# Optimization experiments

Measured on AMD Instinct MI355X. Metric: run time of the kernel, lower is better.

## Reference

```python
import jax, jax.numpy as jnp
import numpy as np

BUCKET_SIZE = 128
HEADS = 8
HEAD_DIM = 64
LOOK_BACKWARD = 1
LOOK_FORWARD = 0  # causal => no look forward
TOKEN_SELF_ATTN_VALUE = -50000.0


def look_around(x, backward, forward, pad_value):
    n = x.shape[1]
    pw = [(0, 0)] * x.ndim
    pw[1] = (backward, forward)
    px = jnp.pad(x, pw, constant_values=pad_value)
    return jnp.concatenate([px[:, i:i + n] for i in range(backward + forward + 1)], axis=2)


def shift(x):
    # relative-shift trick: (..., i, j) -> (..., i, j)
    *lead, i, j = x.shape
    x = jnp.concatenate([x, jnp.zeros((*lead, i, i), x.dtype)], axis=-1)
    l = i + j - 1
    x = x.reshape(*lead, i * (i + j))
    pad = (-x.shape[-1]) % l
    x = jnp.concatenate([x, jnp.zeros((*lead, pad), x.dtype)], axis=-1)
    x = x.reshape(*lead, -1, l)
    return x[..., :i, i - 1:]


def setup_inputs() -> dict:
    key = jax.random.key(0)
    kq, kk, kv, kr = jax.random.split(key, 4)
    B, H, T, E = 2, HEADS, 8192, HEAD_DIM
    q = jax.random.normal(kq, (B, H, T, E), dtype=jnp.float32)
    k = jax.random.normal(kk, (B, H, T, E), dtype=jnp.float32)
    v = jax.random.normal(kv, (B, H, T, E), dtype=jnp.float32)
    rel_weights = jax.random.normal(kr, (2 * BUCKET_SIZE, H, E), dtype=jnp.float32)
    return {"q": q, "k": k, "v": v, "rel_weights": rel_weights}


def reference(q, k, v, rel_weights):
    B, H, T, E = q.shape
    qm = q.reshape(B * H, T, E)
    km = k.reshape(B * H, T, E)
    vm = v.reshape(B * H, T, E)

    # shared_qk: l2-normalize keys (F.normalize with eps=1e-12)
    km = km / jnp.maximum(jnp.linalg.norm(km, axis=-1, keepdims=True), 1e-12)

    buckets = T // BUCKET_SIZE
    bq = qm.reshape(B * H, buckets, BUCKET_SIZE, E)
    bk = km.reshape(B * H, buckets, BUCKET_SIZE, E)
    bv = vm.reshape(B * H, buckets, BUCKET_SIZE, E)

    bk = look_around(bk, LOOK_BACKWARD, LOOK_FORWARD, -1.0)
    bv = look_around(bv, LOOK_BACKWARD, LOOK_FORWARD, -1.0)

    ticker = jnp.arange(T, dtype=q.dtype)
    bq_t = ticker.reshape(1, buckets, BUCKET_SIZE)
    bq_k = look_around(bq_t, LOOK_BACKWARD, LOOK_FORWARD, -1.0)

    scale = E ** -0.5
    dots = jnp.einsum('bnie,bnje->bnij', bq, bk) * scale

    # relative positional bias
    bq5 = bq.reshape(B, H, buckets, BUCKET_SIZE, E)
    emb = jnp.einsum('bhnid,jhd->bhnij', bq5, rel_weights) * scale
    dots = dots + shift(emb).reshape(dots.shape)

    mask_value = -jnp.finfo(dots.dtype).max
    # shared_qk: mask self-attention positions
    self_mask = bq_t[:, :, :, None] == bq_k[:, :, None, :]
    dots = jnp.where(self_mask, TOKEN_SELF_ATTN_VALUE, dots)
    # causal mask
    causal_mask = bq_t[:, :, :, None] < bq_k[:, :, None, :]
    dots = jnp.where(causal_mask, mask_value, dots)
    # look-around padding mask
    pad_mask = (bq_k == -1.0)[:, :, None, :]
    dots = jnp.where(pad_mask, mask_value, dots)

    attn = jax.nn.softmax(dots, axis=-1)
    out = jnp.einsum('bnij,bnje->bnie', attn, bv)
    return out.reshape(B, H, T, E)
```

## Files before the change

### kernel.cpp

```cpp
#include <hip/hip_runtime.h>
#include <hip/hip_bf16.h>
#include <float.h>

#define NHEAD 8

typedef __attribute__((ext_vector_type(8))) short bf16x8;
typedef __attribute__((ext_vector_type(4))) float f32x4;

struct US44 { ushort4 a, b; };

static __device__ __forceinline__ unsigned short bfb(float f) {
    __hip_bfloat16 h = __float2bfloat16(f);
    unsigned short u; __builtin_memcpy(&u, &h, 2); return u;
}
static __device__ __forceinline__ unsigned int pk2(float a, float b) {
    return (unsigned int)bfb(a) | ((unsigned int)bfb(b) << 16);
}
static __device__ __forceinline__ float bf2f_lo(unsigned int u) { return __uint_as_float(u << 16); }
static __device__ __forceinline__ float bf2f_hi(unsigned int u) { return __uint_as_float(u & 0xffff0000u); }

static __device__ __forceinline__ int swz64(int r, int c) {
    return (r << 6) + (c ^ ((r & 7) << 3));
}
static __device__ __forceinline__ int vIdx(int c, int kk) {
    return (c << 8) + (kk ^ ((c & 31) << 2));
}
static __device__ __forceinline__ int pIdx(int wv, int row, int col) {
    const int ch = (col >> 3) ^ (row & 3);
    return (wv * 16 + row) * 40 + ch * 8 + (col & 7);
}

static __device__ __forceinline__ f32x4 mfma16(bf16x8 a, bf16x8 b, f32x4 c) {
    return __builtin_amdgcn_mfma_f32_16x16x32_bf16(a, b, c, 0, 0, 0);
}

__global__ __launch_bounds__(512, 4)
void local_attn_kernel(const float* __restrict__ qg, const float* __restrict__ kg,
                       const float* __restrict__ vg, const float* __restrict__ rwg,
                       float* __restrict__ outg)
{
    __shared__ __align__(16) unsigned short sB[256 * 64];
    __shared__ __align__(16) unsigned short sV[64 * 256];
    __shared__ __align__(16) unsigned short sP[8 * 16 * 40];

    const int tid  = threadIdx.x;
    const int lane = tid & 63;
    const int wv   = tid >> 6;
    const int jl   = lane & 15;
    const int hi   = lane >> 4;

    const int lb = ((blockIdx.x & 7) << 7) + (blockIdx.x >> 3);
    const int bh = lb >> 6;
    const int n  = lb & 63;
    const int h  = bh & 7;

    const float scale = 0.125f;

    const float* Qp = qg + ((size_t)bh * 8192 + (size_t)n * 128) * 64;
    const float* Kp = kg + (size_t)bh * 8192 * 64 + ((long)n - 1) * 128 * 64;
    const float* Vp = vg + (size_t)bh * 8192 * 64 + ((long)n - 1) * 128 * 64;

    const int cr = tid >> 4;
    const int c0 = (tid & 15) << 2;

    #pragma unroll
    for (int pp = 0; pp < 8; ++pp) {
        const int row = pp * 32 + cr;
        f32x4 x = {0.f, 0.f, 0.f, 0.f};
        if (!(n == 0 && row < 128))
            x = *reinterpret_cast<const f32x4*>(Vp + row * 64 + c0);
        #pragma unroll
        for (int q = 0; q < 4; ++q)
            sV[vIdx(c0 + q, row)] = bfb(x[q]);
    }

    #pragma unroll
    for (int pp = 0; pp < 8; ++pp) {
        const int row = pp * 32 + cr;
        f32x4 x = {0.f, 0.f, 0.f, 0.f};
        if (!(n == 0 && row < 128))
            x = *reinterpret_cast<const f32x4*>(Kp + row * 64 + c0);
        float ss = x[0] * x[0] + x[1] * x[1] + x[2] * x[2] + x[3] * x[3];
        ss += __shfl_xor(ss, 1);
        ss += __shfl_xor(ss, 2);
        ss += __shfl_xor(ss, 4);
        ss += __shfl_xor(ss, 8);
        const float rn = 1.0f / fmaxf(sqrtf(ss), 1e-12f);
        ushort4 pkk = make_ushort4(bfb(x[0] * rn), bfb(x[1] * rn),
                                   bfb(x[2] * rn), bfb(x[3] * rn));
        *reinterpret_cast<ushort4*>(&sB[swz64(row, c0)]) = pkk;
    }

    uint2 rwu[8];
    #pragma unroll
    for (int pp = 0; pp < 8; ++pp) {
        const int row = pp * 32 + cr;
        const f32x4 x = *reinterpret_cast<const f32x4*>(rwg + ((size_t)row * NHEAD + h) * 64 + c0);
        rwu[pp] = make_uint2(pk2(x[0], x[1]), pk2(x[2], x[3]));
    }
    #pragma unroll
    for (int pp = 0; pp < 8; ++pp)
        asm volatile("" :: "v"(rwu[pp].x), "v"(rwu[pp].y));

    const int arow = wv * 16 + jl;
    const int kq0  = hi << 3;
    const float* qr = Qp + arow * 64 + kq0;
    const f32x4 qa = *reinterpret_cast<const f32x4*>(qr);
    const f32x4 qb = *reinterpret_cast<const f32x4*>(qr + 4);
    const f32x4 qc = *reinterpret_cast<const f32x4*>(qr + 32);
    const f32x4 qd = *reinterpret_cast<const f32x4*>(qr + 36);
    bf16x8 aq0, aq1;
    #pragma unroll
    for (int q = 0; q < 4; ++q) {
        aq0[q]     = (short)bfb(qa[q] * scale);
        aq0[q + 4] = (short)bfb(qb[q] * scale);
        aq1[q]     = (short)bfb(qc[q] * scale);
        aq1[q + 4] = (short)bfb(qd[q] * scale);
    }

    __syncthreads();

    const int ibase = wv * 16 + (hi << 2);
    const int tMax  = wv + 8;

    f32x4 dots[16] = {};
    __builtin_amdgcn_s_setprio(1);
    #pragma unroll
    for (int t = 0; t < 16; ++t) {
        if (t <= tMax) {
            const int rr = t * 16 + jl;
            const bf16x8 b0 = *reinterpret_cast<const bf16x8*>(&sB[swz64(rr, kq0)]);
            const bf16x8 b1 = *reinterpret_cast<const bf16x8*>(&sB[swz64(rr, 32 + kq0)]);
            f32x4 d = {0.f, 0.f, 0.f, 0.f};
            d = mfma16(aq0, b0, d);
            d = mfma16(aq1, b1, d);
            dots[t] = d;
        }
    }
    __builtin_amdgcn_s_setprio(0);

    __syncthreads();

    #pragma unroll
    for (int pp = 0; pp < 8; ++pp) {
        const int row = pp * 32 + cr;
        *reinterpret_cast<uint2*>(&sB[swz64(row, c0)]) = rwu[pp];
    }

    __syncthreads();

    const int cv0 = 4 * hi + 1, cv1 = 4 * hi + 2, cv2 = 4 * hi + 3, cv3 = 4 * hi + 4;
    const int sl0 = (hi << 4) | ((jl - cv0) & 15);
    const int sl1 = (hi << 4) | ((jl - cv1) & 15);
    const int sl2 = (hi << 4) | ((jl - cv2) & 15);
    const int sl3 = (hi << 4) | ((jl - cv3) & 15);
    const bool g0 = jl >= cv0, g1 = jl >= cv1, g2 = jl >= cv2, g3 = jl >= cv3;

    unsigned int cur01, cur23;
    {
        const int rr = (7 - wv) * 16 + jl;
        const bf16x8 b0 = *reinterpret_cast<const bf16x8*>(&sB[swz64(rr, kq0)]);
        const bf16x8 b1 = *reinterpret_cast<const bf16x8*>(&sB[swz64(rr, 32 + kq0)]);
        f32x4 e = {0.f, 0.f, 0.f, 0.f};
        e = mfma16(aq0, b0, e);
        e = mfma16(aq1, b1, e);
        cur01 = pk2(e[0], e[1]);
        cur23 = pk2(e[2], e[3]);
    }
    unsigned int lo0 = (unsigned int)__shfl((int)cur01, sl0);
    unsigned int lo1 = (unsigned int)__shfl((int)cur01, sl1);
    unsigned int lo2 = (unsigned int)__shfl((int)cur23, sl2);
    unsigned int lo3 = (unsigned int)__shfl((int)cur23, sl3);

    #pragma unroll
    for (int t = 0; t < 16; ++t) {
        if (t <= tMax) {
            unsigned int n01 = 0, n23 = 0;
            const int ts = t + 8 - wv;
            if (ts < 16) {
                const int rr = ts * 16 + jl;
                const bf16x8 b0 = *reinterpret_cast<const bf16x8*>(&sB[swz64(rr, kq0)]);
                const bf16x8 b1 = *reinterpret_cast<const bf16x8*>(&sB[swz64(rr, 32 + kq0)]);
                f32x4 e = {0.f, 0.f, 0.f, 0.f};
                e = mfma16(aq0, b0, e);
                e = mfma16(aq1, b1, e);
                n01 = pk2(e[0], e[1]);
                n23 = pk2(e[2], e[3]);
            }
            const unsigned int h0 = (unsigned int)__shfl((int)n01, sl0);
            const unsigned int h1 = (unsigned int)__shfl((int)n01, sl1);
            const unsigned int h2 = (unsigned int)__shfl((int)n23, sl2);
            const unsigned int h3 = (unsigned int)__shfl((int)n23, sl3);
            dots[t][0] += bf2f_lo(g0 ? h0 : lo0);
            dots[t][1] += bf2f_hi(g1 ? h1 : lo1);
            dots[t][2] += bf2f_lo(g2 ? h2 : lo2);
            dots[t][3] += bf2f_hi(g3 ? h3 : lo3);
            lo0 = h0; lo1 = h1; lo2 = h2; lo3 = h3;
        }
    }

    #pragma unroll
    for (int tt = 8; tt <= 15; ++tt) {
        if (tt == tMax) {
            #pragma unroll
            for (int r = 0; r < 4; ++r) {
                const int dd = 128 + jl - 4 * hi - r;
                float x = dots[tt][r];
                x = (dd == 128) ? -50.0f : x;
                x = (dd > 128) ? -3.0e38f : x;
                dots[tt][r] = x;
            }
        }
    }
    if (n == 0) {
        #pragma unroll
        for (int t = 0; t < 8; ++t)
            #pragma unroll
            for (int r = 0; r < 4; ++r)
                dots[t][r] = -3.0e38f;
    }

    float sm[4] = {0.f, 0.f, 0.f, 0.f};
    #pragma unroll
    for (int t = 0; t < 16; ++t) {
        if (t <= tMax) {
            #pragma unroll
            for (int r = 0; r < 4; ++r) {
                const float pe = __expf(dots[t][r]);
                dots[t][r] = pe;
                sm[r] += pe;
            }
        }
    }
    float rinv[4];
    #pragma unroll
    for (int r = 0; r < 4; ++r) {
        sm[r] += __shfl_xor(sm[r], 1);
        sm[r] += __shfl_xor(sm[r], 2);
        sm[r] += __shfl_xor(sm[r], 4);
        sm[r] += __shfl_xor(sm[r], 8);
        rinv[r] = 1.0f / sm[r];
    }

    f32x4 o[4] = {};
    #pragma unroll
    for (int pv = 0; pv < 8; ++pv) {
        if (2 * pv <= tMax) {
            #pragma unroll
            for (int tt = 0; tt < 2; ++tt) {
                const int t = 2 * pv + tt;
                #pragma unroll
                for (int r = 0; r < 4; ++r) {
                    unsigned short val = 0;
                    if (t <= tMax) val = bfb(dots[t][r]);
                    sP[pIdx(wv, 4 * hi + r, tt * 16 + jl)] = val;
                }
            }
            const bf16x8 pa = *reinterpret_cast<const bf16x8*>(&sP[pIdx(wv, jl, kq0)]);
            __builtin_amdgcn_s_setprio(1);
            #pragma unroll
            for (int ct = 0; ct < 4; ++ct) {
                const int c = ct * 16 + jl;
                const ushort4 v0 = *reinterpret_cast<const ushort4*>(&sV[vIdx(c, pv * 32 + kq0)]);
                const ushort4 v1 = *reinterpret_cast<const ushort4*>(&sV[vIdx(c, pv * 32 + kq0 + 4)]);
                const bf16x8 vb = __builtin_bit_cast(bf16x8, US44{v0, v1});
                o[ct] = mfma16(pa, vb, o[ct]);
            }
            __builtin_amdgcn_s_setprio(0);
        }
    }

    float* Op = outg + ((size_t)bh * 8192 + (size_t)n * 128) * 64;
    #pragma unroll
    for (int ct = 0; ct < 4; ++ct)
        #pragma unroll
        for (int r = 0; r < 4; ++r)
            Op[(ibase + r) * 64 + ct * 16 + jl] = o[ct][r] * rinv[r];
}

extern "C" void kernel_launch(void* const* d_in, const int* in_sizes, int n_in,
                              void* d_out, int out_size, void* d_ws, size_t ws_size,
                              hipStream_t stream) {
    const float* q  = (const float*)d_in[0];
    const float* k  = (const float*)d_in[1];
    const float* v  = (const float*)d_in[2];
    const float* rw = (const float*)d_in[3];
    float* out = (float*)d_out;
    local_attn_kernel<<<dim3(1024), dim3(512), 0, stream>>>(q, k, v, rw, out);
}
```

Before: 48.87 us.

## Process two consecutive buckets per block, reusing shared K/V window and rel weights

Each block now handles two adjacent query buckets, so the grid is halved. The second bucket's look-back K/V half is the first bucket's own K/V and the rel-weight registers are reused, so global loads and normalization per bucket shrink. The next bucket's K is prefetched into registers during the first bucket's softmax, and the V halves are addressed with an XOR phase instead of being copied. In exchange there are fewer blocks (512 on a large GPU), which lowers parallelism and occupancy, and there is more register pressure from the prefetch buffers.

```diff
diff --git a/kernel.cpp b/kernel.cpp
--- a/kernel.cpp
+++ b/kernel.cpp
@@ -49,46 +49,52 @@
     const int jl   = lane & 15;
     const int hi   = lane >> 4;
 
-    const int lb = ((blockIdx.x & 7) << 7) + (blockIdx.x >> 3);
-    const int bh = lb >> 6;
-    const int n  = lb & 63;
-    const int h  = bh & 7;
+    const int bid = blockIdx.x;
+    const int lb  = ((bid & 7) << 6) + (bid >> 3);
+    const int bh  = lb >> 5;
+    const int nb  = (lb & 31) << 1;
+    const int h   = bh & 7;
 
     const float scale = 0.125f;
-
-    const float* Qp = qg + ((size_t)bh * 8192 + (size_t)n * 128) * 64;
-    const float* Kp = kg + (size_t)bh * 8192 * 64 + ((long)n - 1) * 128 * 64;
-    const float* Vp = vg + (size_t)bh * 8192 * 64 + ((long)n - 1) * 128 * 64;
+    const size_t bhOff = (size_t)bh * 8192 * 64;
 
     const int cr = tid >> 4;
     const int c0 = (tid & 15) << 2;
 
-    #pragma unroll
-    for (int pp = 0; pp < 8; ++pp) {
-        const int row = pp * 32 + cr;
-        f32x4 x = {0.f, 0.f, 0.f, 0.f};
-        if (!(n == 0 && row < 128))
-            x = *reinterpret_cast<const f32x4*>(Vp + row * 64 + c0);
-        #pragma unroll
-        for (int q = 0; q < 4; ++q)
-            sV[vIdx(c0 + q, row)] = bfb(x[q]);
-    }
-
-    #pragma unroll
-    for (int pp = 0; pp < 8; ++pp) {
-        const int row = pp * 32 + cr;
-        f32x4 x = {0.f, 0.f, 0.f, 0.f};
-        if (!(n == 0 && row < 128))
-            x = *reinterpret_cast<const f32x4*>(Kp + row * 64 + c0);
-        float ss = x[0] * x[0] + x[1] * x[1] + x[2] * x[2] + x[3] * x[3];
-        ss += __shfl_xor(ss, 1);
-        ss += __shfl_xor(ss, 2);
-        ss += __shfl_xor(ss, 4);
-        ss += __shfl_xor(ss, 8);
-        const float rn = 1.0f / fmaxf(sqrtf(ss), 1e-12f);
-        ushort4 pkk = make_ushort4(bfb(x[0] * rn), bfb(x[1] * rn),
-                                   bfb(x[2] * rn), bfb(x[3] * rn));
-        *reinterpret_cast<ushort4*>(&sB[swz64(row, c0)]) = pkk;
+    const int arow  = wv * 16 + jl;
+    const int kq0   = hi << 3;
+    const int ibase = wv * 16 + (hi << 2);
+    const int tMax  = wv + 8;
+
+    {
+        const float* Vp = vg + bhOff + ((long)nb - 1) * 128 * 64;
+        #pragma unroll
+        for (int pp = 0; pp < 8; ++pp) {
+            const int row = pp * 32 + cr;
+            f32x4 x = {0.f, 0.f, 0.f, 0.f};
+            if (!(nb == 0 && row < 128))
+                x = *reinterpret_cast<const f32x4*>(Vp + row * 64 + c0);
+            #pragma unroll
+            for (int q = 0; q < 4; ++q)
+                sV[vIdx(c0 + q, row)] = bfb(x[q]);
+        }
+        const float* Kp = kg + bhOff + ((long)nb - 1) * 128 * 64;
+        #pragma unroll
+        for (int pp = 0; pp < 8; ++pp) {
+            const int row = pp * 32 + cr;
+            f32x4 x = {0.f, 0.f, 0.f, 0.f};
+            if (!(nb == 0 && row < 128))
+                x = *reinterpret_cast<const f32x4*>(Kp + row * 64 + c0);
+            float ss = x[0] * x[0] + x[1] * x[1] + x[2] * x[2] + x[3] * x[3];
+            ss += __shfl_xor(ss, 1);
+            ss += __shfl_xor(ss, 2);
+            ss += __shfl_xor(ss, 4);
+            ss += __shfl_xor(ss, 8);
+            const float rn = 1.0f / fmaxf(sqrtf(ss), 1e-12f);
+            ushort4 pkk = make_ushort4(bfb(x[0] * rn), bfb(x[1] * rn),
+                                       bfb(x[2] * rn), bfb(x[3] * rn));
+            *reinterpret_cast<ushort4*>(&sB[swz64(row, c0)]) = pkk;
+        }
     }
 
     uint2 rwu[8];
@@ -102,180 +108,259 @@
     for (int pp = 0; pp < 8; ++pp)
         asm volatile("" :: "v"(rwu[pp].x), "v"(rwu[pp].y));
 
-    const int arow = wv * 16 + jl;
-    const int kq0  = hi << 3;
-    const float* qr = Qp + arow * 64 + kq0;
-    const f32x4 qa = *reinterpret_cast<const f32x4*>(qr);
-    const f32x4 qb = *reinterpret_cast<const f32x4*>(qr + 4);
-    const f32x4 qc = *reinterpret_cast<const f32x4*>(qr + 32);
-    const f32x4 qd = *reinterpret_cast<const f32x4*>(qr + 36);
     bf16x8 aq0, aq1;
+    {
+        const float* qr = qg + bhOff + (size_t)nb * 128 * 64 + arow * 64 + kq0;
+        const f32x4 qa = *reinterpret_cast<const f32x4*>(qr);
+        const f32x4 qb = *reinterpret_cast<const f32x4*>(qr + 4);
+        const f32x4 qc = *reinterpret_cast<const f32x4*>(qr + 32);
+        const f32x4 qd = *reinterpret_cast<const f32x4*>(qr + 36);
+        #pragma unroll
+        for (int q = 0; q < 4; ++q) {
+            aq0[q]     = (short)bfb(qa[q] * scale);
+            aq0[q + 4] = (short)bfb(qb[q] * scale);
+            aq1[q]     = (short)bfb(qc[q] * scale);
+            aq1[q + 4] = (short)bfb(qd[q] * scale);
+        }
+    }
+
+    __syncthreads();
+
     #pragma unroll
-    for (int q = 0; q < 4; ++q) {
-        aq0[q]     = (short)bfb(qa[q] * scale);
-        aq0[q + 4] = (short)bfb(qb[q] * scale);
-        aq1[q]     = (short)bfb(qc[q] * scale);
-        aq1[q + 4] = (short)bfb(qd[q] * scale);
-    }
-
-    __syncthreads();
-
-    const int ibase = wv * 16 + (hi << 2);
-    const int tMax  = wv + 8;
-
-    f32x4 dots[16] = {};
-    __builtin_amdgcn_s_setprio(1);
-    #pragma unroll
-    for (int t = 0; t < 16; ++t) {
-        if (t <= tMax) {
-            const int rr = t * 16 + jl;
+    for (int it = 0; it < 2; ++it) {
+        const int n   = nb + it;
+        const int vph = it << 7;
+
+        f32x4 dots[16] = {};
+        __builtin_amdgcn_s_setprio(1);
+        #pragma unroll
+        for (int t = 0; t < 16; ++t) {
+            if (t <= tMax) {
+                const int rr = t * 16 + jl;
+                const bf16x8 b0 = *reinterpret_cast<const bf16x8*>(&sB[swz64(rr, kq0)]);
+                const bf16x8 b1 = *reinterpret_cast<const bf16x8*>(&sB[swz64(rr, 32 + kq0)]);
+                f32x4 d = {0.f, 0.f, 0.f, 0.f};
+                d = mfma16(aq0, b0, d);
+                d = mfma16(aq1, b1, d);
+                dots[t] = d;
+            }
+        }
+        __builtin_amdgcn_s_setprio(0);
+
+        __syncthreads();
+
+        #pragma unroll
+        for (int pp = 0; pp < 8; ++pp) {
+            const int row = pp * 32 + cr;
+            *reinterpret_cast<uint2*>(&sB[swz64(row, c0)]) = rwu[pp];
+        }
+
+        __syncthreads();
+
+        const int cv0 = 4 * hi + 1, cv1 = 4 * hi + 2, cv2 = 4 * hi + 3, cv3 = 4 * hi + 4;
+        const int sl0 = (hi << 4) | ((jl - cv0) & 15);
+        const int sl1 = (hi << 4) | ((jl - cv1) & 15);
+        const int sl2 = (hi << 4) | ((jl - cv2) & 15);
+        const int sl3 = (hi << 4) | ((jl - cv3) & 15);
+        const bool g0 = jl >= cv0, g1 = jl >= cv1, g2 = jl >= cv2, g3 = jl >= cv3;
+
+        unsigned int cur01, cur23;
+        {
+            const int rr = (7 - wv) * 16 + jl;
             const bf16x8 b0 = *reinterpret_cast<const bf16x8*>(&sB[swz64(rr, kq0)]);
             const bf16x8 b1 = *reinterpret_cast<const bf16x8*>(&sB[swz64(rr, 32 + kq0)]);
-            f32x4 d = {0.f, 0.f, 0.f, 0.f};
-            d = mfma16(aq0, b0, d);
-            d = mfma16(aq1, b1, d);
-            dots[t] = d;
+            f32x4 e = {0.f, 0.f, 0.f, 0.f};
+            e = mfma16(aq0, b0, e);
+            e = mfma16(aq1, b1, e);
+            cur01 = pk2(e[0], e[1]);
+            cur23 = pk2(e[2], e[3]);
+        }
+        unsigned int lo0 = (unsigned int)__shfl((int)cur01, sl0);
+        unsigned int lo1 = (unsigned int)__shfl((int)cur01, sl1);
+        unsigned int lo2 = (unsigned int)__shfl((int)cur23, sl2);
+        unsigned int lo3 = (unsigned int)__shfl((int)cur23, sl3);
+
+        #pragma unroll
+        for (int t = 0; t < 16; ++t) {
+            if (t <= tMax) {
+                unsigned int n01 = 0, n23 = 0;
+                const int ts = t + 8 - wv;
+                if (ts < 16) {
+                    const int rr = ts * 16 + jl;
+                    const bf16x8 b0 = *reinterpret_cast<const bf16x8*>(&sB[swz64(rr, kq0)]);
+                    const bf16x8 b1 = *reinterpret_cast<const bf16x8*>(&sB[swz64(rr, 32 + kq0)]);
+                    f32x4 e = {0.f, 0.f, 0.f, 0.f};
+                    e = mfma16(aq0, b0, e);
+                    e = mfma16(aq1, b1, e);
+                    n01 = pk2(e[0], e[1]);
+                    n23 = pk2(e[2], e[3]);
+                }
+                const unsigned int h0 = (unsigned int)__shfl((int)n01, sl0);
+                const unsigned int h1 = (unsigned int)__shfl((int)n01, sl1);
+                const unsigned int h2 = (unsigned int)__shfl((int)n23, sl2);
+                const unsigned int h3 = (unsigned int)__shfl((int)n23, sl3);
+                dots[t][0] += bf2f_lo(g0 ? h0 : lo0);
+                dots[t][1] += bf2f_hi(g1 ? h1 : lo1);
+                dots[t][2] += bf2f_lo(g2 ? h2 : lo2);
+                dots[t][3] += bf2f_hi(g3 ? h3 : lo3);
+                lo0 = h0; lo1 = h1; lo2 = h2; lo3 = h3;
+            }
+        }
+
+        #pragma unroll
+        for (int tt = 8; tt <= 15; ++tt) {
+            if (tt == tMax) {
+                #pragma unroll
+                for (int r = 0; r < 4; ++r) {
+                    const int dd = 128 + jl - 4 * hi - r;
+                    float x = dots[tt][r];
+                    x = (dd == 128) ? -50.0f : x;
+                    x = (dd > 128) ? -3.0e38f : x;
+                    dots[tt][r] = x;
+                }
+            }
+        }
+        if (n == 0) {
+            #pragma unroll
+            for (int t = 0; t < 8; ++t)
+                #pragma unroll
+                for (int r = 0; r < 4; ++r)
+                    dots[t][r] = -3.0e38f;
+        }
+
+        float sm[4] = {0.f, 0.f, 0.f, 0.f};
+        #pragma unroll
+        for (int t = 0; t < 16; ++t) {
+            if (t <= tMax) {
+                #pragma unroll
+                for (int r = 0; r < 4; ++r) {
+                    const float pe = __expf(dots[t][r]);
+                    dots[t][r] = pe;
+                    sm[r] += pe;
+                }
+            }
+        }
+        float rinv[4];
+        #pragma unroll
+        for (int r = 0; r < 4; ++r) {
+            sm[r] += __shfl_xor(sm[r], 1);
+            sm[r] += __shfl_xor(sm[r], 2);
+            sm[r] += __shfl_xor(sm[r], 4);
+            sm[r] += __shfl_xor(sm[r], 8);
+            rinv[r] = 1.0f / sm[r];
+        }
+
+        f32x4 kregA[4];
+        if (it == 0) {
+            const float* Kn = kg + bhOff + (size_t)nb * 128 * 64;
+            #pragma unroll
+            for (int p = 0; p < 4; ++p)
+                kregA[p] = *reinterpret_cast<const f32x4*>(Kn + (p * 32 + cr) * 64 + c0);
+            #pragma unroll
+            for (int p = 0; p < 4; ++p)
+                asm volatile("" :: "v"(kregA[p][0]), "v"(kregA[p][1]), "v"(kregA[p][2]), "v"(kregA[p][3]));
+        }
+
+        f32x4 o[4] = {};
+        #pragma unroll
+        for (int pv = 0; pv < 8; ++pv) {
+            if (2 * pv <= tMax) {
+                #pragma unroll
+                for (int tt = 0; tt < 2; ++tt) {
+                    const int t = 2 * pv + tt;
+                    #pragma unroll
+                    for (int r = 0; r < 4; ++r) {
+                        unsigned short val = 0;
+                        if (t <= tMax) val = bfb(dots[t][r]);
+                        sP[pIdx(wv, 4 * hi + r, tt * 16 + jl)] = val;
+                    }
+                }
+                const bf16x8 pa = *reinterpret_cast<const bf16x8*>(&sP[pIdx(wv, jl, kq0)]);
+                __builtin_amdgcn_s_setprio(1);
+                #pragma unroll
+                for (int ct = 0; ct < 4; ++ct) {
+                    const int c = ct * 16 + jl;
+                    const ushort4 v0 = *reinterpret_cast<const ushort4*>(&sV[vIdx(c, (pv * 32 + kq0) ^ vph)]);
+                    const ushort4 v1 = *reinterpret_cast<const ushort4*>(&sV[vIdx(c, (pv * 32 + kq0 + 4) ^ vph)]);
+                    const bf16x8 vb = __builtin_bit_cast(bf16x8, US44{v0, v1});
+                    o[ct] = mfma16(pa, vb, o[ct]);
+                }
+                __builtin_amdgcn_s_setprio(0);
+            }
+        }
+
+        float* Op = outg + ((size_t)bh * 8192 + (size_t)n * 128) * 64;
+        #pragma unroll
+        for (int ct = 0; ct < 4; ++ct)
+            #pragma unroll
+            for (int r = 0; r < 4; ++r)
+                Op[(ibase + r) * 64 + ct * 16 + jl] = o[ct][r] * rinv[r];
+
+        if (it == 0) {
+            __syncthreads();
+
+            f32x4 kregB[4], vregN[4], qreg[4];
+            const float* Kn = kg + bhOff + (size_t)nb * 128 * 64;
+            #pragma unroll
+            for (int p = 0; p < 4; ++p)
+                kregB[p] = *reinterpret_cast<const f32x4*>(Kn + ((p + 4) * 32 + cr) * 64 + c0);
+            const float* Vn = vg + bhOff + (size_t)(nb + 1) * 128 * 64;
+            #pragma unroll
+            for (int p = 0; p < 4; ++p)
+                vregN[p] = *reinterpret_cast<const f32x4*>(Vn + (p * 32 + cr) * 64 + c0);
+            const float* qr2 = qg + bhOff + (size_t)(nb + 1) * 128 * 64 + arow * 64 + kq0;
+            qreg[0] = *reinterpret_cast<const f32x4*>(qr2);
+            qreg[1] = *reinterpret_cast<const f32x4*>(qr2 + 4);
+            qreg[2] = *reinterpret_cast<const f32x4*>(qr2 + 32);
+            qreg[3] = *reinterpret_cast<const f32x4*>(qr2 + 36);
+
+            #pragma unroll
+            for (int p = 0; p < 4; ++p) {
+                const int row = p * 32 + cr;
+                const f32x4 x = kregA[p];
+                float ss = x[0] * x[0] + x[1] * x[1] + x[2] * x[2] + x[3] * x[3];
+                ss += __shfl_xor(ss, 1);
+                ss += __shfl_xor(ss, 2);
+                ss += __shfl_xor(ss, 4);
+                ss += __shfl_xor(ss, 8);
+                const float rn = 1.0f / fmaxf(sqrtf(ss), 1e-12f);
+                ushort4 pkk = make_ushort4(bfb(x[0] * rn), bfb(x[1] * rn),
+                                           bfb(x[2] * rn), bfb(x[3] * rn));
+                *reinterpret_cast<ushort4*>(&sB[swz64(row, c0)]) = pkk;
+            }
+            #pragma unroll
+            for (int p = 0; p < 4; ++p) {
+                const int row = (p + 4) * 32 + cr;
+                const f32x4 x = kregB[p];
+                float ss = x[0] * x[0] + x[1] * x[1] + x[2] * x[2] + x[3] * x[3];
+                ss += __shfl_xor(ss, 1);
+                ss += __shfl_xor(ss, 2);
+                ss += __shfl_xor(ss, 4);
+                ss += __shfl_xor(ss, 8);
+                const float rn = 1.0f / fmaxf(sqrtf(ss), 1e-12f);
+                ushort4 pkk = make_ushort4(bfb(x[0] * rn), bfb(x[1] * rn),
+                                           bfb(x[2] * rn), bfb(x[3] * rn));
+                *reinterpret_cast<ushort4*>(&sB[swz64(row, c0)]) = pkk;
+            }
+            #pragma unroll
+            for (int p = 0; p < 4; ++p) {
+                const int row2 = p * 32 + cr;
+                const f32x4 x = vregN[p];
+                #pragma unroll
+                for (int q = 0; q < 4; ++q)
+                    sV[vIdx(c0 + q, row2)] = bfb(x[q]);
+            }
+            #pragma unroll
+            for (int q = 0; q < 4; ++q) {
+                aq0[q]     = (short)bfb(qreg[0][q] * scale);
+                aq0[q + 4] = (short)bfb(qreg[1][q] * scale);
+                aq1[q]     = (short)bfb(qreg[2][q] * scale);
+                aq1[q + 4] = (short)bfb(qreg[3][q] * scale);
+            }
+
+            __syncthreads();
         }
     }
-    __builtin_amdgcn_s_setprio(0);
-
-    __syncthreads();
-
-    #pragma unroll
-    for (int pp = 0; pp < 8; ++pp) {
-        const int row = pp * 32 + cr;
-        *reinterpret_cast<uint2*>(&sB[swz64(row, c0)]) = rwu[pp];
-    }
-
-    __syncthreads();
-
-    const int cv0 = 4 * hi + 1, cv1 = 4 * hi + 2, cv2 = 4 * hi + 3, cv3 = 4 * hi + 4;
-    const int sl0 = (hi << 4) | ((jl - cv0) & 15);
-    const int sl1 = (hi << 4) | ((jl - cv1) & 15);
-    const int sl2 = (hi << 4) | ((jl - cv2) & 15);
-    const int sl3 = (hi << 4) | ((jl - cv3) & 15);
-    const bool g0 = jl >= cv0, g1 = jl >= cv1, g2 = jl >= cv2, g3 = jl >= cv3;
-
-    unsigned int cur01, cur23;
-    {
-        const int rr = (7 - wv) * 16 + jl;
-        const bf16x8 b0 = *reinterpret_cast<const bf16x8*>(&sB[swz64(rr, kq0)]);
-        const bf16x8 b1 = *reinterpret_cast<const bf16x8*>(&sB[swz64(rr, 32 + kq0)]);
-        f32x4 e = {0.f, 0.f, 0.f, 0.f};
-        e = mfma16(aq0, b0, e);
-        e = mfma16(aq1, b1, e);
-        cur01 = pk2(e[0], e[1]);
-        cur23 = pk2(e[2], e[3]);
-    }
-    unsigned int lo0 = (unsigned int)__shfl((int)cur01, sl0);
-    unsigned int lo1 = (unsigned int)__shfl((int)cur01, sl1);
-    unsigned int lo2 = (unsigned int)__shfl((int)cur23, sl2);
-    unsigned int lo3 = (unsigned int)__shfl((int)cur23, sl3);
-
-    #pragma unroll
-    for (int t = 0; t < 16; ++t) {
-        if (t <= tMax) {
-            unsigned int n01 = 0, n23 = 0;
-            const int ts = t + 8 - wv;
-            if (ts < 16) {
-                const int rr = ts * 16 + jl;
-                const bf16x8 b0 = *reinterpret_cast<const bf16x8*>(&sB[swz64(rr, kq0)]);
-                const bf16x8 b1 = *reinterpret_cast<const bf16x8*>(&sB[swz64(rr, 32 + kq0)]);
-                f32x4 e = {0.f, 0.f, 0.f, 0.f};
-                e = mfma16(aq0, b0, e);
-                e = mfma16(aq1, b1, e);
-                n01 = pk2(e[0], e[1]);
-                n23 = pk2(e[2], e[3]);
-            }
-            const unsigned int h0 = (unsigned int)__shfl((int)n01, sl0);
-            const unsigned int h1 = (unsigned int)__shfl((int)n01, sl1);
-            const unsigned int h2 = (unsigned int)__shfl((int)n23, sl2);
-            const unsigned int h3 = (unsigned int)__shfl((int)n23, sl3);
-            dots[t][0] += bf2f_lo(g0 ? h0 : lo0);
-            dots[t][1] += bf2f_hi(g1 ? h1 : lo1);
-            dots[t][2] += bf2f_lo(g2 ? h2 : lo2);
-            dots[t][3] += bf2f_hi(g3 ? h3 : lo3);
-            lo0 = h0; lo1 = h1; lo2 = h2; lo3 = h3;
-        }
-    }
-
-    #pragma unroll
-    for (int tt = 8; tt <= 15; ++tt) {
-        if (tt == tMax) {
-            #pragma unroll
-            for (int r = 0; r < 4; ++r) {
-                const int dd = 128 + jl - 4 * hi - r;
-                float x = dots[tt][r];
-                x = (dd == 128) ? -50.0f : x;
-                x = (dd > 128) ? -3.0e38f : x;
-                dots[tt][r] = x;
-            }
-        }
-    }
-    if (n == 0) {
-        #pragma unroll
-        for (int t = 0; t < 8; ++t)
-            #pragma unroll
-            for (int r = 0; r < 4; ++r)
-                dots[t][r] = -3.0e38f;
-    }
-
-    float sm[4] = {0.f, 0.f, 0.f, 0.f};
-    #pragma unroll
-    for (int t = 0; t < 16; ++t) {
-        if (t <= tMax) {
-            #pragma unroll
-            for (int r = 0; r < 4; ++r) {
-                const float pe = __expf(dots[t][r]);
-                dots[t][r] = pe;
-                sm[r] += pe;
-            }
-        }
-    }
-    float rinv[4];
-    #pragma unroll
-    for (int r = 0; r < 4; ++r) {
-        sm[r] += __shfl_xor(sm[r], 1);
-        sm[r] += __shfl_xor(sm[r], 2);
-        sm[r] += __shfl_xor(sm[r], 4);
-        sm[r] += __shfl_xor(sm[r], 8);
-        rinv[r] = 1.0f / sm[r];
-    }
-
-    f32x4 o[4] = {};
-    #pragma unroll
-    for (int pv = 0; pv < 8; ++pv) {
-        if (2 * pv <= tMax) {
-            #pragma unroll
-            for (int tt = 0; tt < 2; ++tt) {
-                const int t = 2 * pv + tt;
-                #pragma unroll
-                for (int r = 0; r < 4; ++r) {
-                    unsigned short val = 0;
-                    if (t <= tMax) val = bfb(dots[t][r]);
-                    sP[pIdx(wv, 4 * hi + r, tt * 16 + jl)] = val;
-                }
-            }
-            const bf16x8 pa = *reinterpret_cast<const bf16x8*>(&sP[pIdx(wv, jl, kq0)]);
-            __builtin_amdgcn_s_setprio(1);
-            #pragma unroll
-            for (int ct = 0; ct < 4; ++ct) {
-                const int c = ct * 16 + jl;
-                const ushort4 v0 = *reinterpret_cast<const ushort4*>(&sV[vIdx(c, pv * 32 + kq0)]);
-                const ushort4 v1 = *reinterpret_cast<const ushort4*>(&sV[vIdx(c, pv * 32 + kq0 + 4)]);
-                const bf16x8 vb = __builtin_bit_cast(bf16x8, US44{v0, v1});
-                o[ct] = mfma16(pa, vb, o[ct]);
-            }
-            __builtin_amdgcn_s_setprio(0);
-        }
-    }
-
-    float* Op = outg + ((size_t)bh * 8192 + (size_t)n * 128) * 64;
-    #pragma unroll
-    for (int ct = 0; ct < 4; ++ct)
-        #pragma unroll
-        for (int r = 0; r < 4; ++r)
-            Op[(ibase + r) * 64 + ct * 16 + jl] = o[ct][r] * rinv[r];
 }
 
 extern "C" void kernel_launch(void* const* d_in, const int* in_sizes, int n_in,
@@ -286,5 +371,5 @@
     const float* v  = (const float*)d_in[2];
     const float* rw = (const float*)d_in[3];
     float* out = (float*)d_out;
-    local_attn_kernel<<<dim3(1024), dim3(512), 0, stream>>>(q, k, v, rw, out);
-}
+    local_attn_kernel<<<dim3(512), dim3(512), 0, stream>>>(q, k, v, rw, out);
+}
```

New measurement: 98.39 us. 101% more time.

## Fuse QK and rel-pos passes, stage V in registers, reuse K buffer

Applied to the files above, without the earlier changes.

The rel-pos weights now get their own shared buffer, so the QK dots and the relative-embedding MFMAs run in a single fused loop instead of two passes separated by barriers. V is loaded column-wise into registers as packed bf16 and written into the freed K buffer only after softmax. That lets the V tile use 16-byte reads with an 8-element swizzle instead of pairs of 8-byte reads. The cost is higher register pressure (32 floats, then 16 packed words, held across the attention phase) and the loss of the setprio hint on the QK loop; the per-thread strided V global loads are also less coalesced.

```diff
diff --git a/kernel.cpp b/kernel.cpp
--- a/kernel.cpp
+++ b/kernel.cpp
@@ -7,8 +7,6 @@
 typedef __attribute__((ext_vector_type(8))) short bf16x8;
 typedef __attribute__((ext_vector_type(4))) float f32x4;
 
-struct US44 { ushort4 a, b; };
-
 static __device__ __forceinline__ unsigned short bfb(float f) {
     __hip_bfloat16 h = __float2bfloat16(f);
     unsigned short u; __builtin_memcpy(&u, &h, 2); return u;
@@ -23,7 +21,7 @@
     return (r << 6) + (c ^ ((r & 7) << 3));
 }
 static __device__ __forceinline__ int vIdx(int c, int kk) {
-    return (c << 8) + (kk ^ ((c & 31) << 2));
+    return (c << 8) + (kk ^ ((c & 31) << 3));
 }
 static __device__ __forceinline__ int pIdx(int wv, int row, int col) {
     const int ch = (col >> 3) ^ (row & 3);
@@ -40,7 +38,7 @@
                        float* __restrict__ outg)
 {
     __shared__ __align__(16) unsigned short sB[256 * 64];
-    __shared__ __align__(16) unsigned short sV[64 * 256];
+    __shared__ __align__(16) unsigned short sRW[256 * 64];
     __shared__ __align__(16) unsigned short sP[8 * 16 * 40];
 
     const int tid  = threadIdx.x;
@@ -55,24 +53,22 @@
     const int h  = bh & 7;
 
     const float scale = 0.125f;
-
-    const float* Qp = qg + ((size_t)bh * 8192 + (size_t)n * 128) * 64;
-    const float* Kp = kg + (size_t)bh * 8192 * 64 + ((long)n - 1) * 128 * 64;
-    const float* Vp = vg + (size_t)bh * 8192 * 64 + ((long)n - 1) * 128 * 64;
+    const size_t bhOff = (size_t)bh * 8192 * 64;
+
+    const float* Qp = qg + bhOff + (size_t)n * 128 * 64;
+    const float* Kp = kg + bhOff + ((long)n - 1) * 128 * 64;
+    const float* Vp = vg + bhOff + ((long)n - 1) * 128 * 64;
 
     const int cr = tid >> 4;
     const int c0 = (tid & 15) << 2;
 
-    #pragma unroll
-    for (int pp = 0; pp < 8; ++pp) {
-        const int row = pp * 32 + cr;
-        f32x4 x = {0.f, 0.f, 0.f, 0.f};
-        if (!(n == 0 && row < 128))
-            x = *reinterpret_cast<const f32x4*>(Vp + row * 64 + c0);
-        #pragma unroll
-        for (int q = 0; q < 4; ++q)
-            sV[vIdx(c0 + q, row)] = bfb(x[q]);
-    }
+    const int vc  = tid & 63;
+    const int vkb = (tid >> 6) << 5;
+    const bool vzero = (n == 0 && vkb < 128);
+    float vx[32];
+    #pragma unroll
+    for (int u = 0; u < 32; ++u)
+        vx[u] = vzero ? 0.f : Vp[(vkb + u) * 64 + vc];
 
     #pragma unroll
     for (int pp = 0; pp < 8; ++pp) {
@@ -91,16 +87,13 @@
         *reinterpret_cast<ushort4*>(&sB[swz64(row, c0)]) = pkk;
     }
 
-    uint2 rwu[8];
     #pragma unroll
     for (int pp = 0; pp < 8; ++pp) {
         const int row = pp * 32 + cr;
         const f32x4 x = *reinterpret_cast<const f32x4*>(rwg + ((size_t)row * NHEAD + h) * 64 + c0);
-        rwu[pp] = make_uint2(pk2(x[0], x[1]), pk2(x[2], x[3]));
-    }
-    #pragma unroll
-    for (int pp = 0; pp < 8; ++pp)
-        asm volatile("" :: "v"(rwu[pp].x), "v"(rwu[pp].y));
+        ushort4 pkw = make_ushort4(bfb(x[0]), bfb(x[1]), bfb(x[2]), bfb(x[3]));
+        *reinterpret_cast<ushort4*>(&sRW[swz64(row, c0)]) = pkw;
+    }
 
     const int arow = wv * 16 + jl;
     const int kq0  = hi << 3;
@@ -118,13 +111,43 @@
         aq1[q + 4] = (short)bfb(qd[q] * scale);
     }
 
+    unsigned int vpk[16];
+    #pragma unroll
+    for (int u = 0; u < 16; ++u)
+        vpk[u] = pk2(vx[2 * u], vx[2 * u + 1]);
+    #pragma unroll
+    for (int u = 0; u < 16; ++u)
+        asm volatile("" :: "v"(vpk[u]));
+
     __syncthreads();
 
     const int ibase = wv * 16 + (hi << 2);
     const int tMax  = wv + 8;
 
+    const int cv0 = 4 * hi + 1, cv1 = 4 * hi + 2, cv2 = 4 * hi + 3, cv3 = 4 * hi + 4;
+    const int sl0 = (hi << 4) | ((jl - cv0) & 15);
+    const int sl1 = (hi << 4) | ((jl - cv1) & 15);
+    const int sl2 = (hi << 4) | ((jl - cv2) & 15);
+    const int sl3 = (hi << 4) | ((jl - cv3) & 15);
+    const bool g0 = jl >= cv0, g1 = jl >= cv1, g2 = jl >= cv2, g3 = jl >= cv3;
+
+    unsigned int cur01, cur23;
+    {
+        const int rr = (7 - wv) * 16 + jl;
+        const bf16x8 b0 = *reinterpret_cast<const bf16x8*>(&sRW[swz64(rr, kq0)]);
+        const bf16x8 b1 = *reinterpret_cast<const bf16x8*>(&sRW[swz64(rr, 32 + kq0)]);
+        f32x4 e = {0.f, 0.f, 0.f, 0.f};
+        e = mfma16(aq0, b0, e);
+        e = mfma16(aq1, b1, e);
+        cur01 = pk2(e[0], e[1]);
+        cur23 = pk2(e[2], e[3]);
+    }
+    unsigned int lo0 = (unsigned int)__shfl((int)cur01, sl0);
+    unsigned int lo1 = (unsigned int)__shfl((int)cur01, sl1);
+    unsigned int lo2 = (unsigned int)__shfl((int)cur23, sl2);
+    unsigned int lo3 = (unsigned int)__shfl((int)cur23, sl3);
+
     f32x4 dots[16] = {};
-    __builtin_amdgcn_s_setprio(1);
     #pragma unroll
     for (int t = 0; t < 16; ++t) {
         if (t <= tMax) {
@@ -134,56 +157,15 @@
             f32x4 d = {0.f, 0.f, 0.f, 0.f};
             d = mfma16(aq0, b0, d);
             d = mfma16(aq1, b1, d);
-            dots[t] = d;
-        }
-    }
-    __builtin_amdgcn_s_setprio(0);
-
-    __syncthreads();
-
-    #pragma unroll
-    for (int pp = 0; pp < 8; ++pp) {
-        const int row = pp * 32 + cr;
-        *reinterpret_cast<uint2*>(&sB[swz64(row, c0)]) = rwu[pp];
-    }
-
-    __syncthreads();
-
-    const int cv0 = 4 * hi + 1, cv1 = 4 * hi + 2, cv2 = 4 * hi + 3, cv3 = 4 * hi + 4;
-    const int sl0 = (hi << 4) | ((jl - cv0) & 15);
-    const int sl1 = (hi << 4) | ((jl - cv1) & 15);
-    const int sl2 = (hi << 4) | ((jl - cv2) & 15);
-    const int sl3 = (hi << 4) | ((jl - cv3) & 15);
-    const bool g0 = jl >= cv0, g1 = jl >= cv1, g2 = jl >= cv2, g3 = jl >= cv3;
-
-    unsigned int cur01, cur23;
-    {
-        const int rr = (7 - wv) * 16 + jl;
-        const bf16x8 b0 = *reinterpret_cast<const bf16x8*>(&sB[swz64(rr, kq0)]);
-        const bf16x8 b1 = *reinterpret_cast<const bf16x8*>(&sB[swz64(rr, 32 + kq0)]);
-        f32x4 e = {0.f, 0.f, 0.f, 0.f};
-        e = mfma16(aq0, b0, e);
-        e = mfma16(aq1, b1, e);
-        cur01 = pk2(e[0], e[1]);
-        cur23 = pk2(e[2], e[3]);
-    }
-    unsigned int lo0 = (unsigned int)__shfl((int)cur01, sl0);
-    unsigned int lo1 = (unsigned int)__shfl((int)cur01, sl1);
-    unsigned int lo2 = (unsigned int)__shfl((int)cur23, sl2);
-    unsigned int lo3 = (unsigned int)__shfl((int)cur23, sl3);
-
-    #pragma unroll
-    for (int t = 0; t < 16; ++t) {
-        if (t <= tMax) {
             unsigned int n01 = 0, n23 = 0;
             const int ts = t + 8 - wv;
             if (ts < 16) {
-                const int rr = ts * 16 + jl;
-                const bf16x8 b0 = *reinterpret_cast<const bf16x8*>(&sB[swz64(rr, kq0)]);
-                const bf16x8 b1 = *reinterpret_cast<const bf16x8*>(&sB[swz64(rr, 32 + kq0)]);
+                const int rr2 = ts * 16 + jl;
+                const bf16x8 e0 = *reinterpret_cast<const bf16x8*>(&sRW[swz64(rr2, kq0)]);
+                const bf16x8 e1 = *reinterpret_cast<const bf16x8*>(&sRW[swz64(rr2, 32 + kq0)]);
                 f32x4 e = {0.f, 0.f, 0.f, 0.f};
-                e = mfma16(aq0, b0, e);
-                e = mfma16(aq1, b1, e);
+                e = mfma16(aq0, e0, e);
+                e = mfma16(aq1, e1, e);
                 n01 = pk2(e[0], e[1]);
                 n23 = pk2(e[2], e[3]);
             }
@@ -191,10 +173,11 @@
             const unsigned int h1 = (unsigned int)__shfl((int)n01, sl1);
             const unsigned int h2 = (unsigned int)__shfl((int)n23, sl2);
             const unsigned int h3 = (unsigned int)__shfl((int)n23, sl3);
-            dots[t][0] += bf2f_lo(g0 ? h0 : lo0);
-            dots[t][1] += bf2f_hi(g1 ? h1 : lo1);
-            dots[t][2] += bf2f_lo(g2 ? h2 : lo2);
-            dots[t][3] += bf2f_hi(g3 ? h3 : lo3);
+            d[0] += bf2f_lo(g0 ? h0 : lo0);
+            d[1] += bf2f_hi(g1 ? h1 : lo1);
+            d[2] += bf2f_lo(g2 ? h2 : lo2);
+            d[3] += bf2f_hi(g3 ? h3 : lo3);
+            dots[t] = d;
             lo0 = h0; lo1 = h1; lo2 = h2; lo3 = h3;
         }
     }
@@ -241,6 +224,17 @@
         sm[r] += __shfl_xor(sm[r], 8);
         rinv[r] = 1.0f / sm[r];
     }
+
+    __syncthreads();
+
+    #pragma unroll
+    for (int w4 = 0; w4 < 4; ++w4) {
+        const uint4 w = make_uint4(vpk[4 * w4], vpk[4 * w4 + 1],
+                                   vpk[4 * w4 + 2], vpk[4 * w4 + 3]);
+        *reinterpret_cast<uint4*>(&sB[vIdx(vc, vkb + 8 * w4)]) = w;
+    }
+
+    __syncthreads();
 
     f32x4 o[4] = {};
     #pragma unroll
@@ -260,17 +254,14 @@
             __builtin_amdgcn_s_setprio(1);
             #pragma unroll
             for (int ct = 0; ct < 4; ++ct) {
-                const int c = ct * 16 + jl;
-                const ushort4 v0 = *reinterpret_cast<const ushort4*>(&sV[vIdx(c, pv * 32 + kq0)]);
-                const ushort4 v1 = *reinterpret_cast<const ushort4*>(&sV[vIdx(c, pv * 32 + kq0 + 4)]);
-                const bf16x8 vb = __builtin_bit_cast(bf16x8, US44{v0, v1});
+                const bf16x8 vb = *reinterpret_cast<const bf16x8*>(&sB[vIdx(ct * 16 + jl, pv * 32 + kq0)]);
                 o[ct] = mfma16(pa, vb, o[ct]);
             }
             __builtin_amdgcn_s_setprio(0);
         }
     }
 
-    float* Op = outg + ((size_t)bh * 8192 + (size_t)n * 128) * 64;
+    float* Op = outg + bhOff + (size_t)n * 128 * 64;
     #pragma unroll
     for (int ct = 0; ct < 4; ++ct)
         #pragma unroll
```

Result: slower. 60.53 us (+23.8%).
